# Kernel tuning notes

Hardware: AMD Instinct MI355X
Metric: run time of the kernel (lower is better)

## Reference

```python
import jax, jax.numpy as jnp
import numpy as np

N = 100000       # nodes
E = 1000000      # edges
NFEAT = 128
NHID = 256
NCLASS = 40
THRESHOLD = 0.1
EPS = 1e-8


def setup_inputs() -> dict:
    key = jax.random.key(0)
    k = jax.random.split(key, 5)
    x = jax.random.normal(k[0], (N, NFEAT), dtype=jnp.float32)
    row = jax.random.randint(k[1], (E,), 0, N)
    col = jax.random.randint(k[2], (E,), 0, N)
    W1 = jax.random.normal(k[3], (NFEAT, NHID), dtype=jnp.float32) / np.sqrt(NFEAT).astype(np.float32)
    b1 = jnp.zeros((NHID,), jnp.float32)
    W2 = jax.random.normal(k[4], (NHID, NCLASS), dtype=jnp.float32) / np.sqrt(NHID).astype(np.float32)
    b2 = jnp.zeros((NCLASS,), jnp.float32)
    return {"x": x, "row": row, "col": col, "W1": W1, "b1": b1, "W2": W2, "b2": b2}


def _att_coef(feat, row, col, prev_mask=None):
    # per-edge cosine similarity (F.cosine_similarity semantics, eps=1e-8)
    nrm = jnp.maximum(jnp.linalg.norm(feat, axis=1), EPS)  # [N]
    dots = jnp.sum(feat[row] * feat[col], axis=1)          # [E] gather-heavy
    sims = dots / (nrm[row] * nrm[col])
    mask = (sims >= THRESHOLD) & (row != col)
    if prev_mask is not None:
        # edges dropped by a previous att_coef no longer exist in the adj
        mask = mask & prev_mask
    # torch.no_grad in original -> weights are constants
    w = jax.lax.stop_gradient(jnp.where(mask, sims, 0.0))
    return w, mask


def _gcn_conv(x, row, col, w, W, b):
    # PyG GCNConv(add_self_loops=True, normalize=True) with edge weights w.
    # Zero-weight edges are exactly equivalent to removed edges.
    h = x @ W                                             # [N, out]
    deg = jnp.zeros((N,), h.dtype).at[row].add(w) + 1.0   # + self-loop weight 1
    dinv = jax.lax.rsqrt(deg)
    norm = dinv[row] * w * dinv[col]                      # [E]
    out = jnp.zeros((N, h.shape[1]), h.dtype).at[row].add(norm[:, None] * h[col])
    out = out + (dinv * dinv)[:, None] * h                # self-loop contribution
    return out + b


def reference(x, row, col, W1, b1, W2, b2):
    w1, m1 = _att_coef(x, row, col)
    h = _gcn_conv(x, row, col, w1, W1, b1)
    h = jax.nn.relu(h)
    # dropout in eval mode -> identity
    w2, _ = _att_coef(h, row, col, prev_mask=m1)
    out = _gcn_conv(h, row, col, w2, W2, b2)
    return out
```

## Files before the change

### kernel.cpp

```cpp
#include <hip/hip_runtime.h>
#include <hip/hip_bf16.h>
#include <hip/hip_fp16.h>

#define NFEAT 128
#define NHID  256
#define NCLASS 40
#define THRESH 0.1f
#define FEPS   1e-8f
#define GUARD2 4e-3f
#define NSTRIPE 384

typedef _Float16 v2h __attribute__((ext_vector_type(2)));
typedef _Float16 v8h __attribute__((ext_vector_type(8)));
typedef float f32x4 __attribute__((ext_vector_type(4)));

__device__ __forceinline__ float dot2acc(unsigned int a, unsigned int b, float s) {
#if __has_builtin(__builtin_amdgcn_fdot2)
    return __builtin_amdgcn_fdot2(__builtin_bit_cast(v2h, a),
                                  __builtin_bit_cast(v2h, b), s, false);
#else
    float2 fa = __half22float2(__builtin_bit_cast(__half2, a));
    float2 fb = __half22float2(__builtin_bit_cast(__half2, b));
    return s + fa.x * fb.x + fa.y * fb.y;
#endif
}

__device__ __forceinline__ int dot4acc(int a, int b, int acc) {
#if __has_builtin(__builtin_amdgcn_sdot4)
    return __builtin_amdgcn_sdot4(a, b, acc, false);
#else
#pragma unroll
    for (int k = 0; k < 4; ++k) {
        int av = (a << (24 - 8 * k)) >> 24;
        int bv = (b << (24 - 8 * k)) >> 24;
        acc += av * bv;
    }
    return acc;
#endif
}

__device__ __forceinline__ float waveSum(float v) {
#pragma unroll
    for (int off = 32; off > 0; off >>= 1) v += __shfl_xor(v, off, 64);
    return v;
}

__device__ __forceinline__ float waveMax(float v) {
#pragma unroll
    for (int off = 32; off > 0; off >>= 1) v = fmaxf(v, __shfl_xor(v, off, 64));
    return v;
}

__global__ void k_prep(const float* __restrict__ x,
                       signed char* __restrict__ xq, signed char* __restrict__ xql,
                       float4* __restrict__ meta,
                       float* __restrict__ nrm, float* __restrict__ deg,
                       float* __restrict__ deg2,
                       int* __restrict__ counts, float* __restrict__ nrmsq, int N) {
    int r = (blockIdx.x * blockDim.x + threadIdx.x) >> 6;
    int lane = threadIdx.x & 63;
    if (r >= N) return;
    float2 a = ((const float2*)(x + (size_t)r * NFEAT))[lane];
    float s = waveSum(a.x * a.x + a.y * a.y);
    float nr = fmaxf(sqrtf(s), FEPS);
    float inv = 1.0f / nr;
    float xn0 = a.x * inv, xn1 = a.y * inv;
    float m = waveMax(fmaxf(fabsf(xn0), fabsf(xn1)));
    float t = (m > 0.f) ? 127.f / m : 0.f;
    float sc = m * (1.0f / 127.f);
    int q0 = __float2int_rn(xn0 * t), q1 = __float2int_rn(xn1 * t);
    q0 = max(-127, min(127, q0));
    q1 = max(-127, min(127, q1));
    char2 pk; pk.x = (signed char)q0; pk.y = (signed char)q1;
    ((char2*)(xq + (size_t)r * NFEAT))[lane] = pk;
    float rq = (m > 0.f) ? 256.0f / sc : 0.f;
    int l0 = __float2int_rn((xn0 - sc * (float)q0) * rq);
    int l1 = __float2int_rn((xn1 - sc * (float)q1) * rq);
    l0 = max(-128, min(127, l0));
    l1 = max(-128, min(127, l1));
    char2 pl; pl.x = (signed char)l0; pl.y = (signed char)l1;
    ((char2*)(xql + (size_t)r * NFEAT))[lane] = pl;
    float asum = waveSum((float)(abs(q0) + abs(q1)));
    float axn  = waveSum(fabsf(xn0) + fabsf(xn1));
    if (lane == 0) {
        meta[r] = make_float4(sc, 0.5f * asum + 33.0f, axn, 0.0f);
        nrm[r] = nr;
        deg[r] = 0.0f;
        deg2[r] = 0.0f;
        counts[r] = 0;
        nrmsq[r] = 0.0f;
    }
}

__global__ void k_w1frag(const float* __restrict__ W1f, v8h* __restrict__ w1x) {
    int id = blockIdx.x * 256 + threadIdx.x;
    int frag = id >> 6, lane = id & 63;
    int kb = frag >> 4, ct = frag & 15;
    int kbase = kb * 32 + (lane >> 4) * 8;
    int n = ct * 16 + (lane & 15);
    v8h v;
#pragma unroll
    for (int j = 0; j < 8; ++j)
        v[j] = (_Float16)W1f[(size_t)(kbase + j) * NHID + n];
    w1x[id] = v;
}

__global__ void k_w2frag(const float* __restrict__ W2f, v8h* __restrict__ w2x) {
    int id = blockIdx.x * 256 + threadIdx.x;
    if (id >= 3072) return;
    int part = (id >= 1536) ? 1 : 0;
    int fid = id - part * 1536;
    int frag = fid >> 6, lane = fid & 63;
    int kb = frag / 3, ct = frag % 3;
    int kbase = kb * 32 + (lane >> 4) * 8;
    int n = ct * 16 + (lane & 15);
    v8h v;
#pragma unroll
    for (int j = 0; j < 8; ++j) {
        float wv = (n < NCLASS) ? W2f[(size_t)(kbase + j) * NCLASS + n] : 0.0f;
        _Float16 hi = (_Float16)wv;
        v[j] = part ? (_Float16)(wv - (float)hi) : hi;
    }
    w2x[id] = v;
}

__global__ void k_att1(const float* __restrict__ xf,
                       const signed char* __restrict__ xq,
                       const signed char* __restrict__ xql,
                       const float4* __restrict__ meta,
                       const int* __restrict__ row, const int* __restrict__ col,
                       const float* __restrict__ nrm,
                       float* __restrict__ w1, float* __restrict__ deg,
                       int* __restrict__ counts, int E) {
    int wid = (blockIdx.x * blockDim.x + threadIdx.x) >> 6;
    int lane = threadIdx.x & 63;
    int l4 = lane & 3;
    int e = wid * 16 + (lane >> 2);
    if (e >= E) return;
    int r = row[e], c = col[e];
    const int4* qra = (const int4*)(xq + (size_t)r * NFEAT);
    const int4* qca = (const int4*)(xq + (size_t)c * NFEAT);
    int4 qa0 = qra[l4 * 2], qa1 = qra[l4 * 2 + 1];
    int4 qb0 = qca[l4 * 2], qb1 = qca[l4 * 2 + 1];
    int d = 0;
    d = dot4acc(qa0.x, qb0.x, d); d = dot4acc(qa0.y, qb0.y, d);
    d = dot4acc(qa0.z, qb0.z, d); d = dot4acc(qa0.w, qb0.w, d);
    d = dot4acc(qa1.x, qb1.x, d); d = dot4acc(qa1.y, qb1.y, d);
    d = dot4acc(qa1.z, qb1.z, d); d = dot4acc(qa1.w, qb1.w, d);
    d += __shfl_xor(d, 1, 64);
    d += __shfl_xor(d, 2, 64);
    float4 mr = meta[r], mc = meta[c];
    float ub = mr.x * mc.x * ((float)d + mr.y + mc.y);
    float sims = 0.0f;
    bool alive = (ub >= THRESH - 1e-5f);
    if (alive) {
        const int4* lra = (const int4*)(xql + (size_t)r * NFEAT);
        const int4* lca = (const int4*)(xql + (size_t)c * NFEAT);
        int4 la0 = lra[l4 * 2], la1 = lra[l4 * 2 + 1];
        int4 lb0 = lca[l4 * 2], lb1 = lca[l4 * 2 + 1];
        int dll = 0, dx = 0;
        dll = dot4acc(la0.x, lb0.x, dll); dll = dot4acc(la0.y, lb0.y, dll);
        dll = dot4acc(la0.z, lb0.z, dll); dll = dot4acc(la0.w, lb0.w, dll);
        dll = dot4acc(la1.x, lb1.x, dll); dll = dot4acc(la1.y, lb1.y, dll);
        dll = dot4acc(la1.z, lb1.z, dll); dll = dot4acc(la1.w, lb1.w, dll);
        dx = dot4acc(qa0.x, lb0.x, dx); dx = dot4acc(qa0.y, lb0.y, dx);
        dx = dot4acc(qa0.z, lb0.z, dx); dx = dot4acc(qa0.w, lb0.w, dx);
        dx = dot4acc(qa1.x, lb1.x, dx); dx = dot4acc(qa1.y, lb1.y, dx);
        dx = dot4acc(qa1.z, lb1.z, dx); dx = dot4acc(qa1.w, lb1.w, dx);
        dx = dot4acc(la0.x, qb0.x, dx); dx = dot4acc(la0.y, qb0.y, dx);
        dx = dot4acc(la0.z, qb0.z, dx); dx = dot4acc(la0.w, qb0.w, dx);
        dx = dot4acc(la1.x, qb1.x, dx); dx = dot4acc(la1.y, qb1.y, dx);
        dx = dot4acc(la1.z, qb1.z, dx); dx = dot4acc(la1.w, qb1.w, dx);
        int conf = dx * 256 + dll;
        conf += __shfl_xor(conf, 1, 64);
        conf += __shfl_xor(conf, 2, 64);
        float ss = mr.x * mc.x;
        sims = ss * ((float)d + (float)conf * (1.0f / 65536.f));
        float errB = (mr.x * mc.z + mc.x * mr.z) * (1.0f / 256.f) + ss * 0.01f + 2e-5f;
        if (__builtin_expect(fabsf(sims - THRESH) < errB, 0)) {
            const float4* fr = (const float4*)(xf + (size_t)r * NFEAT);
            const float4* fc = (const float4*)(xf + (size_t)c * NFEAT);
            float s2 = 0.f;
#pragma unroll
            for (int j = 0; j < 8; ++j) {
                float4 av = fr[l4 + 4 * j], bv = fc[l4 + 4 * j];
                s2 += av.x * bv.x + av.y * bv.y + av.z * bv.z + av.w * bv.w;
            }
            s2 += __shfl_xor(s2, 1, 64);
            s2 += __shfl_xor(s2, 2, 64);
            sims = s2 / (nrm[r] * nrm[c]);
        }
    }
    if (l4 == 0) {
        float w = (alive && sims >= THRESH && r != c) ? sims : 0.0f;
        w1[e] = w;
        if (w != 0.0f) {
            unsafeAtomicAdd(&deg[r], w);
            atomicAdd(&counts[r], 1);
        }
    }
}

__global__ __launch_bounds__(256) void k_scan1(const int* __restrict__ counts,
                                               int* __restrict__ rowptr,
                                               int* __restrict__ bsum, int N) {
    __shared__ int tmp[256];
    int t = threadIdx.x, i = blockIdx.x * 256 + t;
    int v = (i < N) ? counts[i] : 0;
    tmp[t] = v;
    __syncthreads();
    for (int off = 1; off < 256; off <<= 1) {
        int add = (t >= off) ? tmp[t - off] : 0;
        __syncthreads();
        tmp[t] += add;
        __syncthreads();
    }
    if (i < N) rowptr[i] = tmp[t] - v;
    if (t == 255) bsum[blockIdx.x] = tmp[t];
}

__global__ __launch_bounds__(512) void k_scan2(int* __restrict__ bsum, int nb) {
    __shared__ int tmp[512];
    int t = threadIdx.x;
    int v = (t < nb) ? bsum[t] : 0;
    tmp[t] = v;
    __syncthreads();
    for (int off = 1; off < 512; off <<= 1) {
        int add = (t >= off) ? tmp[t - off] : 0;
        __syncthreads();
        tmp[t] += add;
        __syncthreads();
    }
    if (t < nb) bsum[t] = tmp[t] - v;
}

__global__ void k_scan3(int* __restrict__ rowptr, const int* __restrict__ bsum, int N) {
    int i = blockIdx.x * 256 + threadIdx.x;
    if (i < N) rowptr[i] += bsum[blockIdx.x];
}

__global__ void k_fill(const int* __restrict__ row, const int* __restrict__ col,
                       const float* __restrict__ wbuf, const float* __restrict__ deg,
                       int* __restrict__ rowptr, int2* __restrict__ edata,
                       int* __restrict__ esrc, int E) {
    int e = blockIdx.x * blockDim.x + threadIdx.x;
    if (e >= E) return;
    float w = wbuf[e];
    if (w == 0.0f) return;
    int r = row[e], c = col[e];
    float dr = 1.0f / sqrtf(1.0f + deg[r]);
    float dc = 1.0f / sqrtf(1.0f + deg[c]);
    float nm = dr * w * dc;
    int pos = atomicAdd(&rowptr[r], 1);
    edata[pos] = make_int2(c, __float_as_int(nm));
    esrc[pos] = r;
}

__global__ void k_gather1(const float* __restrict__ xf, const int* __restrict__ rowptr,
                          const int* __restrict__ counts, const float* __restrict__ deg,
                          const int2* __restrict__ edata, float* __restrict__ xagg, int N) {
    int tid = blockIdx.x * blockDim.x + threadIdx.x;
    int r = tid >> 3;
    int l = tid & 7;
    if (r >= N) return;
    int cnt = counts[r];
    int start = rowptr[r] - cnt;
    float d = 1.0f / sqrtf(1.0f + deg[r]);
    float dd = d * d;
    const float4* xr = (const float4*)(xf + (size_t)r * NFEAT) + l * 4;
    float4 c0, c1, c2, c3;
    {
        float4 a0 = xr[0], a1 = xr[1], a2 = xr[2], a3 = xr[3];
        c0 = make_float4(dd * a0.x, dd * a0.y, dd * a0.z, dd * a0.w);
        c1 = make_float4(dd * a1.x, dd * a1.y, dd * a1.z, dd * a1.w);
        c2 = make_float4(dd * a2.x, dd * a2.y, dd * a2.z, dd * a2.w);
        c3 = make_float4(dd * a3.x, dd * a3.y, dd * a3.z, dd * a3.w);
    }
    for (int k = 0; k < cnt; ++k) {
        int2 ed = edata[start + k];
        float nm = __int_as_float(ed.y);
        const float4* xc = (const float4*)(xf + (size_t)ed.x * NFEAT) + l * 4;
        float4 b0 = xc[0], b1 = xc[1], b2 = xc[2], b3 = xc[3];
        c0.x += nm * b0.x; c0.y += nm * b0.y; c0.z += nm * b0.z; c0.w += nm * b0.w;
        c1.x += nm * b1.x; c1.y += nm * b1.y; c1.z += nm * b1.z; c1.w += nm * b1.w;
        c2.x += nm * b2.x; c2.y += nm * b2.y; c2.z += nm * b2.z; c2.w += nm * b2.w;
        c3.x += nm * b3.x; c3.y += nm * b3.y; c3.z += nm * b3.z; c3.w += nm * b3.w;
    }
    float4* xo = (float4*)(xagg + (size_t)r * NFEAT) + l * 4;
    xo[0] = c0; xo[1] = c1; xo[2] = c2; xo[3] = c3;
}

__global__ __launch_bounds__(256) void k_gemm1h(const float* __restrict__ xagg,
                                                const v8h* __restrict__ w1x,
                                                const float* __restrict__ b1f,
                                                __half* __restrict__ hh16,
                                                float* __restrict__ nrmsq, int N) {
    __shared__ __half2 xsh[64][68];
    __shared__ v8h bsh[4][8][64];
    int tid = threadIdx.x;
    int ch = blockIdx.x & 1;
    int stripe = blockIdx.x >> 1;

#pragma unroll
    for (int it = 0; it < 8; ++it) {
        int id = it * 256 + tid;
        int lane = id & 63, fr = id >> 6;
        int kb = fr >> 3, ctl = fr & 7;
        bsh[kb][ctl][lane] = w1x[(size_t)(kb * 16 + ch * 8 + ctl) * 64 + lane];
    }

    int w = tid >> 6, lane = tid & 63;
    int c = lane & 15, q = lane >> 4;
    int nb = w * 16;

    int T = (N + 63) >> 6;
    for (int t = stripe; t < T; t += NSTRIPE) {
        int i0 = t * 64;
        __syncthreads();

#pragma unroll
        for (int it = 0; it < 16; ++it) {
            int idx = it * 256 + tid;
            int n = idx >> 6, kq = idx & 63;
            int i = i0 + n;
            float2 v = make_float2(0.f, 0.f);
            if (i < N) v = ((const float2*)(xagg + (size_t)i * NFEAT))[kq];
            xsh[n][kq] = __floats2half2_rn(v.x, v.y);
        }
        __syncthreads();

        f32x4 acc[8];
#pragma unroll
        for (int ct = 0; ct < 8; ++ct) acc[ct] = (f32x4){0.f, 0.f, 0.f, 0.f};

#pragma unroll
        for (int kb = 0; kb < 4; ++kb) {
            v8h a = *((const v8h*)&xsh[nb + c][kb * 16 + q * 4]);
#pragma unroll
            for (int ctl = 0; ctl < 8; ++ctl) {
                acc[ctl] = __builtin_amdgcn_mfma_f32_16x16x32_f16(
                    a, bsh[kb][ctl][lane], acc[ctl], 0, 0, 0);
            }
        }

        float s2[4] = {0.f, 0.f, 0.f, 0.f};
        bool full = (i0 + 64 <= N);
#pragma unroll
        for (int ctl = 0; ctl < 8; ++ctl) {
            int n = (ch * 8 + ctl) * 16 + c;
            float bias = b1f[n];
            f32x4 d = acc[ctl];
#pragma unroll
            for (int reg = 0; reg < 4; ++reg) {
                int node = i0 + nb + q * 4 + reg;
                float v = fmaxf(d[reg] + bias, 0.f);
                s2[reg] += v * v;
                if (full || node < N) hh16[(size_t)node * NHID + n] = __float2half(v);
            }
        }
#pragma unroll
        for (int off = 1; off < 16; off <<= 1) {
#pragma unroll
            for (int reg = 0; reg < 4; ++reg) s2[reg] += __shfl_xor(s2[reg], off, 64);
        }
        if (c == 0) {
            int base = i0 + nb + q * 4;
#pragma unroll
            for (int reg = 0; reg < 4; ++reg)
                if (base + reg < N) unsafeAtomicAdd(&nrmsq[base + reg], s2[reg]);
        }
    }
}

__global__ __launch_bounds__(256) void k_att2e(
        const float* __restrict__ xagg, const float* __restrict__ W1f,
        const float* __restrict__ b1f, const __half2* __restrict__ hh,
        const int* __restrict__ esrc, const int2* __restrict__ edata,
        const float* __restrict__ nrmsq, const int* __restrict__ etot,
        float* __restrict__ w2csr, float* __restrict__ deg2) {
    int lane = threadIdx.x & 63;
    int l8 = lane & 7, g = lane >> 3;
    int wid0 = (blockIdx.x * blockDim.x + threadIdx.x) >> 6;
    int step = (gridDim.x * blockDim.x) >> 3;
    int total = *etot;
    for (int base = wid0 * 8; base < total; base += step) {
        int pos = base + g;
        bool active = (pos < total);
        int r = 0, c = 0;
        float sims = 0.f, inv = 0.f;
        if (active) {
            r = esrc[pos];
            c = edata[pos].x;
            const uint4* hr4 = (const uint4*)(hh + (size_t)r * (NHID / 2));
            const uint4* hc4 = (const uint4*)(hh + (size_t)c * (NHID / 2));
            float s = 0.f;
#pragma unroll
            for (int j = 0; j < 4; ++j) {
                uint4 a = hr4[l8 + 8 * j];
                uint4 b = hc4[l8 + 8 * j];
                s = dot2acc(a.x, b.x, s); s = dot2acc(a.y, b.y, s);
                s = dot2acc(a.z, b.z, s); s = dot2acc(a.w, b.w, s);
            }
            s += __shfl_xor(s, 1, 64);
            s += __shfl_xor(s, 2, 64);
            s += __shfl_xor(s, 4, 64);
            float nr = fmaxf(sqrtf(nrmsq[r]), FEPS);
            float nc = fmaxf(sqrtf(nrmsq[c]), FEPS);
            inv = 1.0f / (nr * nc);
            sims = s * inv;
        }
        unsigned long long gm =
            __ballot(active && l8 == 0 && fabsf(sims - THRESH) < GUARD2);
        while (gm) {
            int src = __ffsll(gm) - 1;
            gm &= gm - 1;
            int rr = __shfl(r, src, 64);
            int cc = __shfl(c, src, 64);
            float invv = __shfl(inv, src, 64);
            int j0 = lane * 4;
            float aR[4], aC[4];
#pragma unroll
            for (int q = 0; q < 4; ++q) { aR[q] = b1f[j0 + q]; aC[q] = b1f[j0 + q]; }
            const float* xr = xagg + (size_t)rr * NFEAT;
            const float* xc = xagg + (size_t)cc * NFEAT;
            for (int kk = 0; kk < NFEAT; ++kk) {
                float vr = xr[kk], vc = xc[kk];
                float4 wv = *((const float4*)(W1f + (size_t)kk * NHID + j0));
                aR[0] += vr * wv.x; aC[0] += vc * wv.x;
                aR[1] += vr * wv.y; aC[1] += vc * wv.y;
                aR[2] += vr * wv.z; aC[2] += vc * wv.z;
                aR[3] += vr * wv.w; aC[3] += vc * wv.w;
            }
            float dp = 0.f;
#pragma unroll
            for (int q = 0; q < 4; ++q)
                dp += fmaxf(aR[q], 0.f) * fmaxf(aC[q], 0.f);
            float se = waveSum(dp) * invv;
            if (lane == src) sims = se;
        }
        if (active && l8 == 0) {
            float w2 = (sims >= THRESH) ? sims : 0.f;
            w2csr[pos] = w2;
            if (w2 != 0.f) unsafeAtomicAdd(&deg2[r], w2);
        }
    }
}

__global__ void k_dinv2(const float* __restrict__ deg2, float* __restrict__ dinv2, int N) {
    int i = blockIdx.x * 256 + threadIdx.x;
    if (i < N) dinv2[i] = 1.0f / sqrtf(1.0f + deg2[i]);
}

__global__ __launch_bounds__(256) void k_gemm2m(const __half2* __restrict__ hh,
                                                const v8h* __restrict__ w2x,
                                                float* __restrict__ g, int N) {
    __shared__ __half2 hs[64][NHID / 2 + 4];
    int tid = threadIdx.x;
    int i0 = blockIdx.x * 64;

#pragma unroll
    for (int it = 0; it < 8; ++it) {
        int idx = it * 256 + tid;
        int n = idx >> 5, kq = idx & 31;
        int i = i0 + n;
        uint4 v = make_uint4(0u, 0u, 0u, 0u);
        if (i < N) v = ((const uint4*)(hh + (size_t)i * (NHID / 2)))[kq];
        *((uint4*)&hs[n][kq * 4]) = v;
    }
    __syncthreads();

    int w = tid >> 6, lane = tid & 63;
    int c = lane & 15, q = lane >> 4;
    int nb = w * 16;

    f32x4 acc[3];
#pragma unroll
    for (int t = 0; t < 3; ++t) acc[t] = (f32x4){0.f, 0.f, 0.f, 0.f};

#pragma unroll
    for (int kb = 0; kb < 8; ++kb) {
        v8h a = *((const v8h*)&hs[nb + c][kb * 16 + q * 4]);
        const v8h* bh = w2x + (size_t)(kb * 3) * 64 + lane;
        const v8h* bl = bh + 1536;
#pragma unroll
        for (int ct = 0; ct < 3; ++ct) {
            acc[ct] = __builtin_amdgcn_mfma_f32_16x16x32_f16(a, bh[ct * 64], acc[ct], 0, 0, 0);
            acc[ct] = __builtin_amdgcn_mfma_f32_16x16x32_f16(a, bl[ct * 64], acc[ct], 0, 0, 0);
        }
    }

    bool full = (i0 + 64 <= N);
#pragma unroll
    for (int ct = 0; ct < 3; ++ct) {
        int cls = ct * 16 + c;
        if (cls < NCLASS) {
            f32x4 d = acc[ct];
#pragma unroll
            for (int reg = 0; reg < 4; ++reg) {
                int node = i0 + nb + q * 4 + reg;
                if (full || node < N) g[(size_t)node * NCLASS + cls] = d[reg];
            }
        }
    }
}

__global__ void k_gather2(const float* __restrict__ g, const int* __restrict__ rowptr,
                          const int* __restrict__ counts, const float* __restrict__ dinv2,
                          const float* __restrict__ b2f, const int2* __restrict__ edata,
                          const float* __restrict__ w2csr, float* __restrict__ out, int N) {
    int tid = blockIdx.x * blockDim.x + threadIdx.x;
    int r = tid >> 3;
    int l = tid & 7;
    if (r >= N) return;
    int cnt = counts[r];
    int start = rowptr[r] - cnt;
    float dr = dinv2[r];
    float drr = dr * dr;
    const float* gr = g + (size_t)r * NCLASS;
    float acc[5];
#pragma unroll
    for (int q = 0; q < 5; ++q) acc[q] = drr * gr[l + 8 * q] + b2f[l + 8 * q];
    for (int k = 0; k < cnt; ++k) {
        int2 ed = edata[start + k];
        float w2 = w2csr[start + k];
        float f = dr * w2 * dinv2[ed.x];
        const float* gc = g + (size_t)ed.x * NCLASS;
#pragma unroll
        for (int q = 0; q < 5; ++q) acc[q] += f * gc[l + 8 * q];
    }
    float* po = out + (size_t)r * NCLASS;
#pragma unroll
    for (int q = 0; q < 5; ++q) po[l + 8 * q] = acc[q];
}

extern "C" void kernel_launch(void* const* d_in, const int* in_sizes, int n_in,
                              void* d_out, int out_size, void* d_ws, size_t ws_size,
                              hipStream_t stream) {
    const float* x  = (const float*)d_in[0];
    const int* row  = (const int*)d_in[1];
    const int* col  = (const int*)d_in[2];
    const float* W1 = (const float*)d_in[3];
    const float* b1 = (const float*)d_in[4];
    const float* W2 = (const float*)d_in[5];
    const float* b2 = (const float*)d_in[6];
    float* out = (float*)d_out;
    const int N = in_sizes[0] / NFEAT;
    const int E = in_sizes[1];

    char* ws = (char*)d_ws;
    size_t off = 0;
    auto alloc = [&](size_t bytes) {
        char* p = ws + off;
        off += (bytes + 255) & ~(size_t)255;
        return p;
    };
    float*   xagg   = (float*)alloc((size_t)N * NFEAT * 4);
    __half2* hh     = (__half2*)alloc((size_t)N * NHID * 2);
    float*   w1buf  = (float*)alloc((size_t)E * 4);
    float*   w2csr  = (float*)alloc((size_t)E * 4);
    int2*    edata  = (int2*)alloc((size_t)E * 8);
    int*     esrc   = (int*)alloc((size_t)E * 4);
    float*   nrm    = (float*)alloc((size_t)N * 4);
    float*   deg    = (float*)alloc((size_t)N * 4);
    float*   dinv2  = (float*)alloc((size_t)N * 4);
    int*     counts = (int*)alloc((size_t)N * 4);
    int*     rowptr = (int*)alloc((size_t)N * 4);
    int*     bsum   = (int*)alloc(512 * 4);
    v8h*     w1x    = (v8h*)alloc(4096 * 16);
    v8h*     w2x    = (v8h*)alloc(3072 * 16);
    float*   nrmsq  = (float*)alloc((size_t)N * 4);
    float*   deg2   = (float*)alloc((size_t)N * 4);
    float*   g      = xagg;
    signed char* xq  = (signed char*)xagg;
    float4*  meta    = (float4*)(xq + (size_t)N * 128);
    signed char* xql = xq + (size_t)N * 144;

    const int e16Blocks = (E + 63) / 64;
    const int eBlocks1 = (E + 255) / 256;
    const int nBlocks4 = (N + 3) / 4;
    const int nBlocks8 = (N + 31) / 32;
    const int scanB    = (N + 255) / 256;

    k_prep<<<nBlocks4, 256, 0, stream>>>(x, xq, xql, meta, nrm, deg, deg2, counts,
                                         nrmsq, N);
    k_w1frag<<<16, 256, 0, stream>>>(W1, w1x);
    k_w2frag<<<12, 256, 0, stream>>>(W2, w2x);
    k_att1<<<e16Blocks, 256, 0, stream>>>(x, xq, xql, meta, row, col, nrm, w1buf, deg,
                                          counts, E);
    k_scan1<<<scanB, 256, 0, stream>>>(counts, rowptr, bsum, N);
    k_scan2<<<1, 512, 0, stream>>>(bsum, scanB);
    k_scan3<<<scanB, 256, 0, stream>>>(rowptr, bsum, N);
    k_fill<<<eBlocks1, 256, 0, stream>>>(row, col, w1buf, deg, rowptr, edata, esrc, E);
    k_gather1<<<nBlocks8, 256, 0, stream>>>(x, rowptr, counts, deg, edata, xagg, N);
    k_gemm1h<<<2 * NSTRIPE, 256, 0, stream>>>(xagg, w1x, b1, (__half*)hh, nrmsq, N);

    k_att2e<<<4096, 256, 0, stream>>>(xagg, W1, b1, hh, esrc, edata, nrmsq,
                                      rowptr + (N - 1), w2csr, deg2);
    k_dinv2<<<scanB, 256, 0, stream>>>(deg2, dinv2, N);
    k_gemm2m<<<(N + 63) / 64, 256, 0, stream>>>(hh, w2x, g, N);
    k_gather2<<<nBlocks8, 256, 0, stream>>>(g, rowptr, counts, dinv2, b2, edata, w2csr,
                                            out, N);
}
```

Measured before the change: 315.7 us.

## Fuse weight-fragment prep into node prep and co-schedule layer-2 GEMM with attention

```diff
diff --git a/kernel.cpp b/kernel.cpp
--- a/kernel.cpp
+++ b/kernel.cpp
@@ -51,77 +51,79 @@
     return v;
 }
 
-__global__ void k_prep(const float* __restrict__ x,
-                       signed char* __restrict__ xq, signed char* __restrict__ xql,
-                       float4* __restrict__ meta,
-                       float* __restrict__ nrm, float* __restrict__ deg,
-                       float* __restrict__ deg2,
-                       int* __restrict__ counts, float* __restrict__ nrmsq, int N) {
-    int r = (blockIdx.x * blockDim.x + threadIdx.x) >> 6;
-    int lane = threadIdx.x & 63;
-    if (r >= N) return;
-    float2 a = ((const float2*)(x + (size_t)r * NFEAT))[lane];
-    float s = waveSum(a.x * a.x + a.y * a.y);
-    float nr = fmaxf(sqrtf(s), FEPS);
-    float inv = 1.0f / nr;
-    float xn0 = a.x * inv, xn1 = a.y * inv;
-    float m = waveMax(fmaxf(fabsf(xn0), fabsf(xn1)));
-    float t = (m > 0.f) ? 127.f / m : 0.f;
-    float sc = m * (1.0f / 127.f);
-    int q0 = __float2int_rn(xn0 * t), q1 = __float2int_rn(xn1 * t);
-    q0 = max(-127, min(127, q0));
-    q1 = max(-127, min(127, q1));
-    char2 pk; pk.x = (signed char)q0; pk.y = (signed char)q1;
-    ((char2*)(xq + (size_t)r * NFEAT))[lane] = pk;
-    float rq = (m > 0.f) ? 256.0f / sc : 0.f;
-    int l0 = __float2int_rn((xn0 - sc * (float)q0) * rq);
-    int l1 = __float2int_rn((xn1 - sc * (float)q1) * rq);
-    l0 = max(-128, min(127, l0));
-    l1 = max(-128, min(127, l1));
-    char2 pl; pl.x = (signed char)l0; pl.y = (signed char)l1;
-    ((char2*)(xql + (size_t)r * NFEAT))[lane] = pl;
-    float asum = waveSum((float)(abs(q0) + abs(q1)));
-    float axn  = waveSum(fabsf(xn0) + fabsf(xn1));
-    if (lane == 0) {
-        meta[r] = make_float4(sc, 0.5f * asum + 33.0f, axn, 0.0f);
-        nrm[r] = nr;
-        deg[r] = 0.0f;
-        deg2[r] = 0.0f;
-        counts[r] = 0;
-        nrmsq[r] = 0.0f;
-    }
-}
-
-__global__ void k_w1frag(const float* __restrict__ W1f, v8h* __restrict__ w1x) {
-    int id = blockIdx.x * 256 + threadIdx.x;
-    int frag = id >> 6, lane = id & 63;
-    int kb = frag >> 4, ct = frag & 15;
-    int kbase = kb * 32 + (lane >> 4) * 8;
-    int n = ct * 16 + (lane & 15);
-    v8h v;
-#pragma unroll
-    for (int j = 0; j < 8; ++j)
-        v[j] = (_Float16)W1f[(size_t)(kbase + j) * NHID + n];
-    w1x[id] = v;
-}
-
-__global__ void k_w2frag(const float* __restrict__ W2f, v8h* __restrict__ w2x) {
-    int id = blockIdx.x * 256 + threadIdx.x;
-    if (id >= 3072) return;
-    int part = (id >= 1536) ? 1 : 0;
-    int fid = id - part * 1536;
-    int frag = fid >> 6, lane = fid & 63;
-    int kb = frag / 3, ct = frag % 3;
-    int kbase = kb * 32 + (lane >> 4) * 8;
-    int n = ct * 16 + (lane & 15);
-    v8h v;
-#pragma unroll
-    for (int j = 0; j < 8; ++j) {
-        float wv = (n < NCLASS) ? W2f[(size_t)(kbase + j) * NCLASS + n] : 0.0f;
-        _Float16 hi = (_Float16)wv;
-        v[j] = part ? (_Float16)(wv - (float)hi) : hi;
-    }
-    w2x[id] = v;
+__global__ void k_prepw(const float* __restrict__ x,
+                        signed char* __restrict__ xq, signed char* __restrict__ xql,
+                        float4* __restrict__ meta,
+                        float* __restrict__ nrm, float* __restrict__ deg,
+                        float* __restrict__ deg2,
+                        int* __restrict__ counts, float* __restrict__ nrmsq,
+                        const float* __restrict__ W1f, v8h* __restrict__ w1x,
+                        const float* __restrict__ W2f, v8h* __restrict__ w2x,
+                        int N, int prepBlocks) {
+    int b = blockIdx.x;
+    int tid = threadIdx.x;
+    if (b < prepBlocks) {
+        int r = (b * 256 + tid) >> 6;
+        int lane = tid & 63;
+        if (r >= N) return;
+        float2 a = ((const float2*)(x + (size_t)r * NFEAT))[lane];
+        float s = waveSum(a.x * a.x + a.y * a.y);
+        float nr = fmaxf(sqrtf(s), FEPS);
+        float inv = 1.0f / nr;
+        float xn0 = a.x * inv, xn1 = a.y * inv;
+        float m = waveMax(fmaxf(fabsf(xn0), fabsf(xn1)));
+        float t = (m > 0.f) ? 127.f / m : 0.f;
+        float sc = m * (1.0f / 127.f);
+        int q0 = __float2int_rn(xn0 * t), q1 = __float2int_rn(xn1 * t);
+        q0 = max(-127, min(127, q0));
+        q1 = max(-127, min(127, q1));
+        char2 pk; pk.x = (signed char)q0; pk.y = (signed char)q1;
+        ((char2*)(xq + (size_t)r * NFEAT))[lane] = pk;
+        float rq = (m > 0.f) ? 256.0f / sc : 0.f;
+        int l0 = __float2int_rn((xn0 - sc * (float)q0) * rq);
+        int l1 = __float2int_rn((xn1 - sc * (float)q1) * rq);
+        l0 = max(-128, min(127, l0));
+        l1 = max(-128, min(127, l1));
+        char2 pl; pl.x = (signed char)l0; pl.y = (signed char)l1;
+        ((char2*)(xql + (size_t)r * NFEAT))[lane] = pl;
+        float asum = waveSum((float)(abs(q0) + abs(q1)));
+        float axn  = waveSum(fabsf(xn0) + fabsf(xn1));
+        if (lane == 0) {
+            meta[r] = make_float4(sc, 0.5f * asum + 33.0f, axn, 0.0f);
+            nrm[r] = nr;
+            deg[r] = 0.0f;
+            deg2[r] = 0.0f;
+            counts[r] = 0;
+            nrmsq[r] = 0.0f;
+        }
+    } else if (b < prepBlocks + 16) {
+        int id = (b - prepBlocks) * 256 + tid;
+        int frag = id >> 6, lane = id & 63;
+        int kb = frag >> 4, ct = frag & 15;
+        int kbase = kb * 32 + (lane >> 4) * 8;
+        int n = ct * 16 + (lane & 15);
+        v8h v;
+#pragma unroll
+        for (int j = 0; j < 8; ++j)
+            v[j] = (_Float16)W1f[(size_t)(kbase + j) * NHID + n];
+        w1x[id] = v;
+    } else {
+        int id = (b - prepBlocks - 16) * 256 + tid;
+        int part = (id >= 1536) ? 1 : 0;
+        int fid = id - part * 1536;
+        int frag = fid >> 6, lane = fid & 63;
+        int kb = frag / 3, ct = frag % 3;
+        int kbase = kb * 32 + (lane >> 4) * 8;
+        int n = ct * 16 + (lane & 15);
+        v8h v;
+#pragma unroll
+        for (int j = 0; j < 8; ++j) {
+            float wv = (n < NCLASS) ? W2f[(size_t)(kbase + j) * NCLASS + n] : 0.0f;
+            _Float16 hi = (_Float16)wv;
+            v[j] = part ? (_Float16)(wv - (float)hi) : hi;
+        }
+        w2x[id] = v;
+    }
 }
 
 __global__ void k_att1(const float* __restrict__ xf,
@@ -372,6 +374,134 @@
     }
 }
 
+__global__ __launch_bounds__(256) void k_l2fused(
+        const __half2* __restrict__ hh, const v8h* __restrict__ w2x,
+        float* __restrict__ g,
+        const float* __restrict__ xagg, const float* __restrict__ W1f,
+        const float* __restrict__ b1f, const int* __restrict__ esrc,
+        const int2* __restrict__ edata, const float* __restrict__ nrmsq,
+        const int* __restrict__ etot, float* __restrict__ w2csr,
+        float* __restrict__ deg2,
+        int gemmBlocks, int N) {
+    __shared__ __half2 hs[64][NHID / 2 + 4];
+    int tid = threadIdx.x;
+    if ((int)blockIdx.x < gemmBlocks) {
+        int i0 = blockIdx.x * 64;
+#pragma unroll
+        for (int it = 0; it < 8; ++it) {
+            int idx = it * 256 + tid;
+            int n = idx >> 5, kq = idx & 31;
+            int i = i0 + n;
+            uint4 v = make_uint4(0u, 0u, 0u, 0u);
+            if (i < N) v = ((const uint4*)(hh + (size_t)i * (NHID / 2)))[kq];
+            *((uint4*)&hs[n][kq * 4]) = v;
+        }
+        __syncthreads();
+
+        int w = tid >> 6, lane = tid & 63;
+        int c = lane & 15, q = lane >> 4;
+        int nb = w * 16;
+
+        f32x4 acc[3];
+#pragma unroll
+        for (int t = 0; t < 3; ++t) acc[t] = (f32x4){0.f, 0.f, 0.f, 0.f};
+
+#pragma unroll
+        for (int kb = 0; kb < 8; ++kb) {
+            v8h a = *((const v8h*)&hs[nb + c][kb * 16 + q * 4]);
+            const v8h* bh = w2x + (size_t)(kb * 3) * 64 + lane;
+            const v8h* bl = bh + 1536;
+#pragma unroll
+            for (int ct = 0; ct < 3; ++ct) {
+                acc[ct] = __builtin_amdgcn_mfma_f32_16x16x32_f16(a, bh[ct * 64], acc[ct], 0, 0, 0);
+                acc[ct] = __builtin_amdgcn_mfma_f32_16x16x32_f16(a, bl[ct * 64], acc[ct], 0, 0, 0);
+            }
+        }
+
+        bool full = (i0 + 64 <= N);
+#pragma unroll
+        for (int ct = 0; ct < 3; ++ct) {
+            int cls = ct * 16 + c;
+            if (cls < NCLASS) {
+                f32x4 d = acc[ct];
+#pragma unroll
+                for (int reg = 0; reg < 4; ++reg) {
+                    int node = i0 + nb + q * 4 + reg;
+                    if (full || node < N) g[(size_t)node * NCLASS + cls] = d[reg];
+                }
+            }
+        }
+    } else {
+        int lane = tid & 63;
+        int l8 = lane & 7, gr8 = lane >> 3;
+        int nb2 = gridDim.x - gemmBlocks;
+        int wid0 = (((int)blockIdx.x - gemmBlocks) * 256 + tid) >> 6;
+        int step = (nb2 * 256) >> 3;
+        int total = *etot;
+        for (int base = wid0 * 8; base < total; base += step) {
+            int pos = base + gr8;
+            bool active = (pos < total);
+            int r = 0, c = 0;
+            float sims = 0.f, inv = 0.f;
+            if (active) {
+                r = esrc[pos];
+                c = edata[pos].x;
+                const uint4* hr4 = (const uint4*)(hh + (size_t)r * (NHID / 2));
+                const uint4* hc4 = (const uint4*)(hh + (size_t)c * (NHID / 2));
+                float s = 0.f;
+#pragma unroll
+                for (int j = 0; j < 4; ++j) {
+                    uint4 a = hr4[l8 + 8 * j];
+                    uint4 b = hc4[l8 + 8 * j];
+                    s = dot2acc(a.x, b.x, s); s = dot2acc(a.y, b.y, s);
+                    s = dot2acc(a.z, b.z, s); s = dot2acc(a.w, b.w, s);
+                }
+                s += __shfl_xor(s, 1, 64);
+                s += __shfl_xor(s, 2, 64);
+                s += __shfl_xor(s, 4, 64);
+                float nr = fmaxf(sqrtf(nrmsq[r]), FEPS);
+                float nc = fmaxf(sqrtf(nrmsq[c]), FEPS);
+                inv = 1.0f / (nr * nc);
+                sims = s * inv;
+            }
+            unsigned long long gm =
+                __ballot(active && l8 == 0 && fabsf(sims - THRESH) < GUARD2);
+            while (gm) {
+                int src = __ffsll(gm) - 1;
+                gm &= gm - 1;
+                int rr = __shfl(r, src, 64);
+                int cc = __shfl(c, src, 64);
+                float invv = __shfl(inv, src, 64);
+                int j0 = lane * 4;
+                float aR[4], aC[4];
+#pragma unroll
+                for (int q = 0; q < 4; ++q) { aR[q] = b1f[j0 + q]; aC[q] = b1f[j0 + q]; }
+                const float* xr = xagg + (size_t)rr * NFEAT;
+                const float* xc = xagg + (size_t)cc * NFEAT;
+                for (int kk = 0; kk < NFEAT; ++kk) {
+                    float vr = xr[kk], vc = xc[kk];
+                    float4 wv = *((const float4*)(W1f + (size_t)kk * NHID + j0));
+                    aR[0] += vr * wv.x; aC[0] += vc * wv.x;
+                    aR[1] += vr * wv.y; aC[1] += vc * wv.y;
+                    aR[2] += vr * wv.z; aC[2] += vc * wv.z;
+                    aR[3] += vr * wv.w; aC[3] += vc * wv.w;
+                }
+                float dp = 0.f;
+#pragma unroll
+                for (int q = 0; q < 4; ++q)
+                    dp += fmaxf(aR[q], 0.f) * fmaxf(aC[q], 0.f);
+                float se = waveSum(dp) * invv;
+                if (lane == src) sims = se;
+            }
+            if (active && l8 == 0) {
+                float w2 = (sims >= THRESH) ? sims : 0.f;
+                w2csr[pos] = w2;
+                if (w2 != 0.f) unsafeAtomicAdd(&deg2[r], w2);
+            }
+        }
+    }
+}
+
 __global__ __launch_bounds__(256) void k_att2e(
         const float* __restrict__ xagg, const float* __restrict__ W1f,
         const float* __restrict__ b1f, const __half2* __restrict__ hh,
@@ -446,18 +576,12 @@
     }
 }
 
-__global__ void k_dinv2(const float* __restrict__ deg2, float* __restrict__ dinv2, int N) {
-    int i = blockIdx.x * 256 + threadIdx.x;
-    if (i < N) dinv2[i] = 1.0f / sqrtf(1.0f + deg2[i]);
-}
-
 __global__ __launch_bounds__(256) void k_gemm2m(const __half2* __restrict__ hh,
                                                 const v8h* __restrict__ w2x,
                                                 float* __restrict__ g, int N) {
     __shared__ __half2 hs[64][NHID / 2 + 4];
     int tid = threadIdx.x;
     int i0 = blockIdx.x * 64;
-
 #pragma unroll
     for (int it = 0; it < 8; ++it) {
         int idx = it * 256 + tid;
@@ -468,15 +592,12 @@
         *((uint4*)&hs[n][kq * 4]) = v;
     }
     __syncthreads();
-
     int w = tid >> 6, lane = tid & 63;
     int c = lane & 15, q = lane >> 4;
     int nb = w * 16;
-
     f32x4 acc[3];
 #pragma unroll
     for (int t = 0; t < 3; ++t) acc[t] = (f32x4){0.f, 0.f, 0.f, 0.f};
-
 #pragma unroll
     for (int kb = 0; kb < 8; ++kb) {
         v8h a = *((const v8h*)&hs[nb + c][kb * 16 + q * 4]);
@@ -488,7 +609,6 @@
             acc[ct] = __builtin_amdgcn_mfma_f32_16x16x32_f16(a, bl[ct * 64], acc[ct], 0, 0, 0);
         }
     }
-
     bool full = (i0 + 64 <= N);
 #pragma unroll
     for (int ct = 0; ct < 3; ++ct) {
@@ -502,6 +622,11 @@
             }
         }
     }
+}
+
+__global__ void k_dinv2(const float* __restrict__ deg2, float* __restrict__ dinv2, int N) {
+    int i = blockIdx.x * 256 + threadIdx.x;
+    if (i < N) dinv2[i] = 1.0f / sqrtf(1.0f + deg2[i]);
 }
 
 __global__ void k_gather2(const float* __restrict__ g, const int* __restrict__ rowptr,
@@ -570,21 +695,23 @@
     v8h*     w2x    = (v8h*)alloc(3072 * 16);
     float*   nrmsq  = (float*)alloc((size_t)N * 4);
     float*   deg2   = (float*)alloc((size_t)N * 4);
-    float*   g      = xagg;
     signed char* xq  = (signed char*)xagg;
     float4*  meta    = (float4*)(xq + (size_t)N * 128);
     signed char* xql = xq + (size_t)N * 144;
+    size_t gBytes = ((size_t)N * NCLASS * 4 + 255) & ~(size_t)255;
+    bool fused = (off + gBytes <= ws_size);
+    float* g = fused ? (float*)alloc(gBytes) : xagg;
 
     const int e16Blocks = (E + 63) / 64;
     const int eBlocks1 = (E + 255) / 256;
     const int nBlocks4 = (N + 3) / 4;
     const int nBlocks8 = (N + 31) / 32;
     const int scanB    = (N + 255) / 256;
-
-    k_prep<<<nBlocks4, 256, 0, stream>>>(x, xq, xql, meta, nrm, deg, deg2, counts,
-                                         nrmsq, N);
-    k_w1frag<<<16, 256, 0, stream>>>(W1, w1x);
-    k_w2frag<<<12, 256, 0, stream>>>(W2, w2x);
+    const int gemmB    = (N + 63) / 64;
+
+    k_prepw<<<nBlocks4 + 28, 256, 0, stream>>>(x, xq, xql, meta, nrm, deg, deg2,
+                                               counts, nrmsq, W1, w1x, W2, w2x,
+                                               N, nBlocks4);
     k_att1<<<e16Blocks, 256, 0, stream>>>(x, xq, xql, meta, row, col, nrm, w1buf, deg,
                                           counts, E);
     k_scan1<<<scanB, 256, 0, stream>>>(counts, rowptr, bsum, N);
@@ -594,10 +721,16 @@
     k_gather1<<<nBlocks8, 256, 0, stream>>>(x, rowptr, counts, deg, edata, xagg, N);
     k_gemm1h<<<2 * NSTRIPE, 256, 0, stream>>>(xagg, w1x, b1, (__half*)hh, nrmsq, N);
 
-    k_att2e<<<4096, 256, 0, stream>>>(xagg, W1, b1, hh, esrc, edata, nrmsq,
-                                      rowptr + (N - 1), w2csr, deg2);
+    if (fused) {
+        k_l2fused<<<gemmB + 4096, 256, 0, stream>>>(hh, w2x, g, xagg, W1, b1, esrc,
+                                                    edata, nrmsq, rowptr + (N - 1),
+                                                    w2csr, deg2, gemmB, N);
+    } else {
+        k_att2e<<<4096, 256, 0, stream>>>(xagg, W1, b1, hh, esrc, edata, nrmsq,
+                                          rowptr + (N - 1), w2csr, deg2);
+        k_gemm2m<<<gemmB, 256, 0, stream>>>(hh, w2x, g, N);
+    }
     k_dinv2<<<scanB, 256, 0, stream>>>(deg2, dinv2, N);
-    k_gemm2m<<<(N + 63) / 64, 256, 0, stream>>>(hh, w2x, g, N);
     k_gather2<<<nBlocks8, 256, 0, stream>>>(g, rowptr, counts, dinv2, b2, edata, w2csr,
                                             out, N);
 }
```

New measurement: 307.2 us. -2.7%, faster.
